# Kernel optimization log

Measured on AMD Instinct MI355X. Metric: run time of the kernel, lower is better.

## Reference

```python
import jax, jax.numpy as jnp
import numpy as np

B, S, T, D, V = 512, 128, 128, 512, 128  # batch, enc len, dec steps (=longest_smi), dim_model, output_size


def setup_inputs() -> dict:
    key = jax.random.key(0)
    ks = jax.random.split(key, 17)
    sc = 0.05
    return {
        "e_all": jax.random.normal(ks[0], (B, S, D), jnp.float32),
        "e_h": jax.random.normal(ks[1], (1, B, D), jnp.float32),
        "e_c": jax.random.normal(ks[2], (1, B, D), jnp.float32),
        "target": jax.random.randint(ks[3], (B, T), 0, T),
        # params (Linear weights stored [in, out], y = x @ W + b)
        "E": jax.random.normal(ks[4], (T, D), jnp.float32) * sc,        # Embedding(longest_smi, D)
        "Wa": jax.random.normal(ks[5], (D, D), jnp.float32) * sc,
        "ba": jnp.zeros((D,), jnp.float32),
        "Ua": jax.random.normal(ks[6], (D, D), jnp.float32) * sc,
        "bu": jnp.zeros((D,), jnp.float32),
        "Va": jax.random.normal(ks[7], (D, 1), jnp.float32) * sc,
        "bv": jnp.zeros((1,), jnp.float32),
        "W_ih": jax.random.normal(ks[8], (2 * D, 4 * D), jnp.float32) * sc,
        "b_ih": jnp.zeros((4 * D,), jnp.float32),
        "W_hh": jax.random.normal(ks[9], (D, 4 * D), jnp.float32) * sc,
        "b_hh": jnp.zeros((4 * D,), jnp.float32),
        "W_out": jax.random.normal(ks[10], (D, V), jnp.float32) * sc,
        "b_out": jnp.zeros((V,), jnp.float32),
    }


def reference(e_all, e_h, e_c, target, E, Wa, ba, Ua, bu, Va, bv,
              W_ih, b_ih, W_hh, b_hh, W_out, b_out):
    Bb = e_all.shape[0]
    # teacher forcing: step 0 input is token 0 (SOS), then target[:, :-1]
    idx = jnp.concatenate([jnp.zeros((Bb, 1), target.dtype), target[:, :-1]], axis=1)  # [B,T]
    emb_all = E[idx]                       # [B,T,D] (dropout is identity in eval)
    keys_proj = e_all @ Ua + bu            # Ua(keys), loop-invariant  [B,S,D]
    h0, c0 = e_h[0], e_c[0]                # [B,D]

    def step(carry, emb):
        h, c = carry
        q = (h + c) @ Wa + ba                                   # [B,D]  Wa(query)
        s = jnp.tanh(q[:, None, :] + keys_proj) @ Va + bv       # [B,S,1]
        w = jax.nn.softmax(s[..., 0], axis=-1)                  # [B,S]
        ctx = jnp.einsum('bs,bsd->bd', w, e_all)                # [B,D]
        x = jnp.concatenate([emb, ctx], axis=-1)                # [B,2D]
        g = x @ W_ih + b_ih + h @ W_hh + b_hh                   # [B,4D], torch gate order i,f,g,o
        i_, f_, g_, o_ = jnp.split(g, 4, axis=-1)
        c2 = jax.nn.sigmoid(f_) * c + jax.nn.sigmoid(i_) * jnp.tanh(g_)
        h2 = jax.nn.sigmoid(o_) * jnp.tanh(c2)
        out = h2 @ W_out + b_out                                # [B,V]
        return (h2, c2), (out, w)

    _, (outs, attns) = jax.lax.scan(step, (h0, c0), jnp.swapaxes(emb_all, 0, 1))
    outputs = jax.nn.log_softmax(jnp.swapaxes(outs, 0, 1), axis=-1)  # [B,T,V]
    cross_attn = jnp.swapaxes(attns, 0, 1)                           # [B,T,S]
    return outputs, cross_attn
```

## Files before the change

kernel.cpp:

```cpp
#include <hip/hip_runtime.h>

#define B_ 512
#define S_ 128
#define T_ 128
#define D_ 512
#define V_ 128
#define LDW 72

typedef __attribute__((ext_vector_type(8))) short s16x8;
typedef __attribute__((ext_vector_type(4))) short s16x4;
typedef __attribute__((ext_vector_type(4))) float f32x4;

__device__ __forceinline__ float b2f(unsigned short h) {
    union { unsigned int u; float f; } x; x.u = ((unsigned int)h) << 16; return x.f;
}
__device__ __forceinline__ unsigned short f2b(float f) {
    union { float f; unsigned int u; } x; x.f = f;
    unsigned int u = x.u; u += 0x7FFFu + ((u >> 16) & 1u);
    return (unsigned short)(u >> 16);
}
#if __has_builtin(__builtin_amdgcn_rcpf)
__device__ __forceinline__ float rcp_f(float x) { return __builtin_amdgcn_rcpf(x); }
#else
__device__ __forceinline__ float rcp_f(float x) { return 1.0f / x; }
#endif
__device__ __forceinline__ float sigm(float x) { return rcp_f(1.0f + __expf(-x)); }
__device__ __forceinline__ float tanh_fast(float x) {
    float e = __expf(2.0f * fabsf(x));
    float r = 1.0f - 2.0f * rcp_f(e + 1.0f);
    return copysignf(r, x);
}
__device__ __forceinline__ float tanh_pade(float x) {
    float t = x * x;
    float num = x * fmaf(t, 105.0f + t, 945.0f);
    float den = fmaf(t, fmaf(t, 15.0f, 420.0f), 945.0f);
    float r = num * rcp_f(den);
    return fminf(1.0f, fmaxf(-1.0f, r));
}

#if __has_builtin(__builtin_amdgcn_cvt_f32_fp8)
__device__ __forceinline__ f32x4 fp8x4_dec(unsigned w) {
    f32x4 r;
    r[0] = __builtin_amdgcn_cvt_f32_fp8(w, 0);
    r[1] = __builtin_amdgcn_cvt_f32_fp8(w, 1);
    r[2] = __builtin_amdgcn_cvt_f32_fp8(w, 2);
    r[3] = __builtin_amdgcn_cvt_f32_fp8(w, 3);
    return r;
}
#else
__device__ __forceinline__ float fp8_dec_sw(unsigned w, int j) {
    unsigned char v = (w >> (8 * j)) & 0xFF;
    unsigned s = v >> 7, e = (v >> 3) & 0xF, m = v & 7;
    float r = (e == 0) ? ldexpf((float)m, -9) : ldexpf((float)(8 + m), (int)e - 10);
    return s ? -r : r;
}
__device__ __forceinline__ f32x4 fp8x4_dec(unsigned w) {
    f32x4 r;
    r[0] = fp8_dec_sw(w, 0); r[1] = fp8_dec_sw(w, 1);
    r[2] = fp8_dec_sw(w, 2); r[3] = fp8_dec_sw(w, 3);
    return r;
}
#endif

#if __has_builtin(__builtin_amdgcn_cvt_pk_fp8_f32)
__device__ __forceinline__ unsigned pk_fp8(float a, float b, float c, float d) {
    int r = 0;
    r = __builtin_amdgcn_cvt_pk_fp8_f32(a, b, r, false);
    r = __builtin_amdgcn_cvt_pk_fp8_f32(c, d, r, true);
    return (unsigned)r;
}
#else
__device__ __forceinline__ unsigned char f32_to_fp8_sw(float x) {
    unsigned s = x < 0.f ? 0x80u : 0u; float a = fabsf(x);
    if (a != a) return (unsigned char)(s | 0x7F);
    if (a >= 448.f) return (unsigned char)(s | 0x7E);
    if (a < 0.001953125f) { int m = (int)rintf(a * 512.0f); return (unsigned char)(s | (m > 7 ? 0x08 : m)); }
    int e; float fr = frexpf(a, &e);
    int m = (int)rintf(fr * 16.0f - 8.0f);
    int ee = e - 1 + 7;
    if (m == 8) { m = 0; ee += 1; }
    if (ee <= 0) { int mm = (int)rintf(a * 512.f); return (unsigned char)(s | (mm > 7 ? 0x08 : mm)); }
    if (ee >= 16) return (unsigned char)(s | 0x7E);
    return (unsigned char)(s | (ee << 3) | m);
}
__device__ __forceinline__ unsigned pk_fp8(float a, float b, float c, float d) {
    return (unsigned)f32_to_fp8_sw(a) | ((unsigned)f32_to_fp8_sw(b) << 8)
         | ((unsigned)f32_to_fp8_sw(c) << 16) | ((unsigned)f32_to_fp8_sw(d) << 24);
}
#endif

struct P {
    const int* target;
    const float* E; const float* bv; const float* ba; const float* bout;
    const short* vab;
    const unsigned char* ea8; const unsigned char* kp8;
    const short* WaT; const short* WehT; const short* WctxT; const short* WoutT;
    const float* bcat;
    short* qbf; short* xeh; short* ctxb; short* gpA; short* gpB;
    short* hcbf; short* h2bf; float* cst;
    float* out_logits; float* out_attn;
};

struct AttnS { float scp[4][64]; float wbuf[S_]; float cpart[4][D_]; };
struct OutS  { short As[64][LDW]; short Bs[128][LDW]; };
struct PG2   { short As[128][LDW]; short Bs[64][LDW]; };
struct GateS { short As[64][LDW]; short Bs[64][LDW]; float gt[64][65]; };
union SharedC { OutS o; PG2 g; };

__device__ __forceinline__ void attn_phase(const P& p, AttnS& sh, int b, int step)
{
    const int t = threadIdx.x, lane = t & 63, wave = t >> 6;
    {
        const int sg = wave & 1, dh = wave >> 1;
        const int s = sg * 64 + lane;
        const unsigned char* kb = p.kp8 + (size_t)b * (S_ * D_);
        const short* qv = p.qbf + (size_t)b * D_;
        float acc = 0.f;
        #pragma unroll 4
        for (int i = 0; i < 16; ++i) {
            int g = dh * 16 + i;
            uint4 kw = *(const uint4*)(kb + ((size_t)g * 128 + s) * 16);
            const short* qg = qv + g * 16;
            const short* vg = p.vab + g * 16;
            s16x8 q0 = *(const s16x8*)(qg), q1 = *(const s16x8*)(qg + 8);
            s16x8 v0 = *(const s16x8*)(vg), v1 = *(const s16x8*)(vg + 8);
            f32x4 ka = fp8x4_dec(kw.x), kb4 = fp8x4_dec(kw.y);
            f32x4 kc = fp8x4_dec(kw.z), kd = fp8x4_dec(kw.w);
            #pragma unroll
            for (int j = 0; j < 4; ++j) {
                acc += tanh_pade(b2f((unsigned short)q0[j])     + ka[j])  * b2f((unsigned short)v0[j]);
                acc += tanh_pade(b2f((unsigned short)q0[4 + j]) + kb4[j]) * b2f((unsigned short)v0[4 + j]);
                acc += tanh_pade(b2f((unsigned short)q1[j])     + kc[j])  * b2f((unsigned short)v1[j]);
                acc += tanh_pade(b2f((unsigned short)q1[4 + j]) + kd[j])  * b2f((unsigned short)v1[4 + j]);
            }
        }
        sh.scp[wave][lane] = acc;
    }
    __syncthreads();
    if (wave == 0) {
        const float bvv = p.bv[0];
        float v0 = sh.scp[0][lane] + sh.scp[2][lane] + bvv;
        float v1 = sh.scp[1][lane] + sh.scp[3][lane] + bvv;
        float m = fmaxf(v0, v1);
        #pragma unroll
        for (int o = 32; o >= 1; o >>= 1) m = fmaxf(m, __shfl_xor(m, o));
        float e0 = __expf(v0 - m), e1 = __expf(v1 - m);
        float su = e0 + e1;
        #pragma unroll
        for (int o = 32; o >= 1; o >>= 1) su += __shfl_xor(su, o);
        float inv = rcp_f(su);
        float w0 = e0 * inv, w1 = e1 * inv;
        sh.wbuf[lane] = w0; sh.wbuf[lane + 64] = w1;
        float* ao = p.out_attn + ((size_t)b * T_ + step) * S_;
        ao[lane] = w0; ao[lane + 64] = w1;
    }
    __syncthreads();
    {
        const int d0 = lane * 8;
        f32x4 aA = {0.f,0.f,0.f,0.f}, aB = {0.f,0.f,0.f,0.f};
        const unsigned char* eb = p.ea8 + (size_t)b * S_ * D_ + d0;
        #pragma unroll 4
        for (int i = 0; i < 32; ++i) {
            int s = wave * 32 + i;
            float wv = sh.wbuf[s];
            uint2 ev = *(const uint2*)(eb + (size_t)s * D_);
            f32x4 ex = fp8x4_dec(ev.x), ey = fp8x4_dec(ev.y);
            #pragma unroll
            for (int j = 0; j < 4; ++j) aA[j] += wv * ex[j];
            #pragma unroll
            for (int j = 0; j < 4; ++j) aB[j] += wv * ey[j];
        }
        *(f32x4*)&sh.cpart[wave][d0]     = aA;
        *(f32x4*)&sh.cpart[wave][d0 + 4] = aB;
    }
    __syncthreads();
    {
        int dd = t * 2;
        float v0 = sh.cpart[0][dd]   + sh.cpart[1][dd]   + sh.cpart[2][dd]   + sh.cpart[3][dd];
        float v1 = sh.cpart[0][dd+1] + sh.cpart[1][dd+1] + sh.cpart[2][dd+1] + sh.cpart[3][dd+1];
        short2 o2; o2.x = (short)f2b(v0); o2.y = (short)f2b(v1);
        *(short2*)(p.ctxb + (size_t)b * D_ + dd) = o2;
    }
}

__device__ __forceinline__ void pgate_phase(const P& p, PG2& sh, int bid2, int koff,
                                            short* __restrict__ gpp, bool addb)
{
    const int t = threadIdx.x, lane = t & 63, wave = t >> 6;
    const int lrow = lane & 15, kq = lane >> 4;
    const int m0 = (bid2 >> 5) * 128, n0 = (bid2 & 31) * 64;
    f32x4 acc[2][4] = {};
    for (int k0 = 0; k0 < 512; k0 += 64) {
        s16x8 va[4], vb[2];
        #pragma unroll
        for (int r = 0; r < 4; ++r) {
            int idx = r * 256 + t, row = idx >> 3, seg = idx & 7;
            va[r] = *(const s16x8*)(p.xeh + (size_t)(m0 + row) * 1024 + koff + k0 + seg * 8);
        }
        #pragma unroll
        for (int r = 0; r < 2; ++r) {
            int idx = r * 256 + t, row = idx >> 3, seg = idx & 7;
            vb[r] = *(const s16x8*)(p.WehT + (size_t)(n0 + row) * 1024 + koff + k0 + seg * 8);
        }
        __syncthreads();
        #pragma unroll
        for (int r = 0; r < 4; ++r) {
            int idx = r * 256 + t, row = idx >> 3, seg = idx & 7;
            *(s16x8*)(&sh.As[row][seg * 8]) = va[r];
        }
        #pragma unroll
        for (int r = 0; r < 2; ++r) {
            int idx = r * 256 + t, row = idx >> 3, seg = idx & 7;
            *(s16x8*)(&sh.Bs[row][seg * 8]) = vb[r];
        }
        __syncthreads();
        #pragma unroll
        for (int kk = 0; kk < 64; kk += 32) {
            s16x8 af[2], bf[4];
            af[0] = *(const s16x8*)(&sh.As[wave * 32 + lrow][kk + kq * 8]);
            af[1] = *(const s16x8*)(&sh.As[wave * 32 + 16 + lrow][kk + kq * 8]);
            #pragma unroll
            for (int f = 0; f < 4; ++f)
                bf[f] = *(const s16x8*)(&sh.Bs[f * 16 + lrow][kk + kq * 8]);
            #pragma unroll
            for (int m2 = 0; m2 < 2; ++m2)
                #pragma unroll
                for (int n2 = 0; n2 < 4; ++n2)
                    acc[m2][n2] = __builtin_amdgcn_mfma_f32_16x16x32_bf16(af[m2], bf[n2], acc[m2][n2], 0, 0, 0);
        }
    }
    #pragma unroll
    for (int m2 = 0; m2 < 2; ++m2)
        #pragma unroll
        for (int n2 = 0; n2 < 4; ++n2) {
            int col = n0 + n2 * 16 + lrow;
            float bvv = addb ? p.bcat[col] : 0.0f;
            #pragma unroll
            for (int j = 0; j < 4; ++j) {
                int row = m0 + wave * 32 + m2 * 16 + kq * 4 + j;
                gpp[(size_t)row * 2048 + col] = (short)f2b(acc[m2][n2][j] + bvv);
            }
        }
}

__device__ __forceinline__ void fgate_phase(const P& p, GateS& sh, int bid, int step)
{
    const int t = threadIdx.x, lane = t & 63, wave = t >> 6;
    const int wr = wave >> 1, wc = wave & 1;
    const int lrow = lane & 15, kq = lane >> 4;
    const int srow = t >> 3, sseg = t & 7;
    const int m0 = (bid >> 5) * 64, n0 = (bid & 31) * 64;
    f32x4 acc[2][2] = {};
    for (int k0 = 0; k0 < 512; k0 += 64) {
        s16x8 va0 = *(const s16x8*)(p.ctxb + (size_t)(m0 + srow) * 512 + k0 + sseg * 8);
        s16x8 va1 = *(const s16x8*)(p.ctxb + (size_t)(m0 + srow + 32) * 512 + k0 + sseg * 8);
        s16x8 vb0 = *(const s16x8*)(p.WctxT + (size_t)(n0 + srow) * 512 + k0 + sseg * 8);
        s16x8 vb1 = *(const s16x8*)(p.WctxT + (size_t)(n0 + srow + 32) * 512 + k0 + sseg * 8);
        __syncthreads();
        *(s16x8*)(&sh.As[srow][sseg * 8]) = va0;
        *(s16x8*)(&sh.As[srow + 32][sseg * 8]) = va1;
        *(s16x8*)(&sh.Bs[srow][sseg * 8]) = vb0;
        *(s16x8*)(&sh.Bs[srow + 32][sseg * 8]) = vb1;
        __syncthreads();
        #pragma unroll
        for (int kk = 0; kk < 64; kk += 32) {
            s16x8 af0 = *(const s16x8*)(&sh.As[wr * 32 + lrow][kk + kq * 8]);
            s16x8 af1 = *(const s16x8*)(&sh.As[wr * 32 + 16 + lrow][kk + kq * 8]);
            s16x8 bf0 = *(const s16x8*)(&sh.Bs[wc * 32 + lrow][kk + kq * 8]);
            s16x8 bf1 = *(const s16x8*)(&sh.Bs[wc * 32 + 16 + lrow][kk + kq * 8]);
            acc[0][0] = __builtin_amdgcn_mfma_f32_16x16x32_bf16(af0, bf0, acc[0][0], 0, 0, 0);
            acc[0][1] = __builtin_amdgcn_mfma_f32_16x16x32_bf16(af0, bf1, acc[0][1], 0, 0, 0);
            acc[1][0] = __builtin_amdgcn_mfma_f32_16x16x32_bf16(af1, bf0, acc[1][0], 0, 0, 0);
            acc[1][1] = __builtin_amdgcn_mfma_f32_16x16x32_bf16(af1, bf1, acc[1][1], 0, 0, 0);
        }
    }
    #pragma unroll
    for (int m2 = 0; m2 < 2; ++m2)
        #pragma unroll
        for (int n2 = 0; n2 < 2; ++n2) {
            int cl = wc * 32 + n2 * 16 + lrow;
            #pragma unroll
            for (int j = 0; j < 4; ++j) {
                int rl = wr * 32 + m2 * 16 + kq * 4 + j;
                size_t gidx = (size_t)(m0 + rl) * 2048 + n0 + cl;
                sh.gt[rl][cl] = acc[m2][n2][j]
                              + b2f((unsigned short)p.gpA[gidx])
                              + b2f((unsigned short)p.gpB[gidx]);
            }
        }
    __syncthreads();
    const int rl4 = t >> 4, dl = t & 15;
    #pragma unroll
    for (int pass = 0; pass < 4; ++pass) {
        int row = pass * 16 + rl4;
        int b = m0 + row;
        int d = (n0 >> 2) + dl;
        float gi = sh.gt[row][dl * 4 + 0];
        float gf = sh.gt[row][dl * 4 + 1];
        float gg = sh.gt[row][dl * 4 + 2];
        float go = sh.gt[row][dl * 4 + 3];
        float cv = p.cst[(size_t)b * D_ + d];
        float c2 = sigm(gf) * cv + sigm(gi) * tanh_fast(gg);
        float h2 = sigm(go) * tanh_fast(c2);
        p.cst[(size_t)b * D_ + d] = c2;
        p.hcbf[(size_t)b * D_ + d] = (short)f2b(h2 + c2);
        p.h2bf[(size_t)b * D_ + d] = (short)f2b(h2);
        p.xeh[(size_t)b * 1024 + 512 + d] = (short)f2b(h2);
        int tok = p.target[b * T_ + step];
        p.xeh[(size_t)b * 1024 + d] = (short)f2b(p.E[(size_t)tok * D_ + d]);
    }
}

__device__ __forceinline__ void q_phase(const P& p, OutS& sh, int bid)
{
    const int t = threadIdx.x, lane = t & 63, wave = t >> 6;
    const int lrow = lane & 15, kq = lane >> 4;
    const int srow = t >> 3, sseg = t & 7;
    const int m0 = (bid >> 4) * 64, n0 = (bid & 15) * 32;
    f32x4 acc0 = {}, acc1 = {};
    for (int k0 = 0; k0 < 512; k0 += 64) {
        s16x8 va0 = *(const s16x8*)(p.hcbf + (size_t)(m0 + srow) * 512 + k0 + sseg * 8);
        s16x8 va1 = *(const s16x8*)(p.hcbf + (size_t)(m0 + srow + 32) * 512 + k0 + sseg * 8);
        int brow = n0 + (srow & 31);
        s16x8 vb0 = *(const s16x8*)(p.WaT + (size_t)brow * 512 + k0 + sseg * 8);
        __syncthreads();
        *(s16x8*)(&sh.As[srow][sseg * 8]) = va0;
        *(s16x8*)(&sh.As[srow + 32][sseg * 8]) = va1;
        if (srow < 32) *(s16x8*)(&sh.Bs[srow][sseg * 8]) = vb0;
        __syncthreads();
        #pragma unroll
        for (int kk = 0; kk < 64; kk += 32) {
            s16x8 af  = *(const s16x8*)(&sh.As[wave * 16 + lrow][kk + kq * 8]);
            s16x8 bf0 = *(const s16x8*)(&sh.Bs[lrow][kk + kq * 8]);
            s16x8 bf1 = *(const s16x8*)(&sh.Bs[16 + lrow][kk + kq * 8]);
            acc0 = __builtin_amdgcn_mfma_f32_16x16x32_bf16(af, bf0, acc0, 0, 0, 0);
            acc1 = __builtin_amdgcn_mfma_f32_16x16x32_bf16(af, bf1, acc1, 0, 0, 0);
        }
    }
    #pragma unroll
    for (int n2 = 0; n2 < 2; ++n2) {
        int col = n0 + n2 * 16 + lrow;
        float bvv = p.ba[col];
        f32x4 av = n2 ? acc1 : acc0;
        #pragma unroll
        for (int j = 0; j < 4; ++j) {
            int row = m0 + wave * 16 + kq * 4 + j;
            p.qbf[(size_t)row * 512 + col] = (short)f2b(av[j] + bvv);
        }
    }
}

__device__ __forceinline__ void out_phase(const P& p, OutS& sh, int obid, int step)
{
    const int t = threadIdx.x, lane = t & 63, wave = t >> 6;
    const int lrow = lane & 15, kq = lane >> 4;
    const int srow = t >> 3, sseg = t & 7;
    const int m0 = obid * 64;
    f32x4 acc[8] = {};
    for (int k0 = 0; k0 < 512; k0 += 64) {
        s16x8 va0 = *(const s16x8*)(p.h2bf + (size_t)(m0 + srow) * 512 + k0 + sseg * 8);
        s16x8 va1 = *(const s16x8*)(p.h2bf + (size_t)(m0 + srow + 32) * 512 + k0 + sseg * 8);
        s16x8 vb[4];
        #pragma unroll
        for (int p4 = 0; p4 < 4; ++p4)
            vb[p4] = *(const s16x8*)(p.WoutT + (size_t)(srow + p4 * 32) * 512 + k0 + sseg * 8);
        __syncthreads();
        *(s16x8*)(&sh.As[srow][sseg * 8]) = va0;
        *(s16x8*)(&sh.As[srow + 32][sseg * 8]) = va1;
        #pragma unroll
        for (int p4 = 0; p4 < 4; ++p4) *(s16x8*)(&sh.Bs[srow + p4 * 32][sseg * 8]) = vb[p4];
        __syncthreads();
        #pragma unroll
        for (int kk = 0; kk < 64; kk += 32) {
            s16x8 a = *(const s16x8*)(&sh.As[wave * 16 + lrow][kk + kq * 8]);
            #pragma unroll
            for (int f = 0; f < 8; ++f) {
                s16x8 b = *(const s16x8*)(&sh.Bs[f * 16 + lrow][kk + kq * 8]);
                acc[f] = __builtin_amdgcn_mfma_f32_16x16x32_bf16(a, b, acc[f], 0, 0, 0);
            }
        }
    }
    float colb[8];
    #pragma unroll
    for (int f = 0; f < 8; ++f) colb[f] = p.bout[f * 16 + lrow];
    #pragma unroll
    for (int j = 0; j < 4; ++j) {
        float v[8]; float mx = -1e30f;
        #pragma unroll
        for (int f = 0; f < 8; ++f) { v[f] = acc[f][j] + colb[f]; mx = fmaxf(mx, v[f]); }
        #pragma unroll
        for (int o = 1; o < 16; o <<= 1) mx = fmaxf(mx, __shfl_xor(mx, o));
        float sum = 0.f;
        #pragma unroll
        for (int f = 0; f < 8; ++f) sum += __expf(v[f] - mx);
        #pragma unroll
        for (int o = 1; o < 16; o <<= 1) sum += __shfl_xor(sum, o);
        float lse = mx + __logf(sum);
        int row = m0 + wave * 16 + kq * 4 + j;
        float* orow = p.out_logits + ((size_t)row * T_ + step) * V_;
        #pragma unroll
        for (int f = 0; f < 8; ++f) orow[f * 16 + lrow] = v[f] - lse;
    }
}

__global__ __launch_bounds__(256, 2) void kA(P p, int step) {
    __shared__ AttnS sh;
    attn_phase(p, sh, blockIdx.x, step);
}
__global__ __launch_bounds__(256, 2) void kB(P p, int step) {
    __shared__ GateS sh;
    fgate_phase(p, sh, blockIdx.x, step);
}
template<bool INIT>
__global__ __launch_bounds__(256, 2) void kC(P p, int step) {
    __shared__ SharedC sh;
    const int bid = blockIdx.x;
    if (bid < 128)       q_phase(p, sh.o, bid);
    else if (bid < 256)  pgate_phase(p, sh.g, bid - 128, 0,   p.gpA, true);
    else if (bid < 384)  pgate_phase(p, sh.g, bid - 256, 512, p.gpB, false);
    else if (!INIT)      out_phase(p, sh.o, bid - 384, step);
}

__global__ __launch_bounds__(256)
void gemm64(const short* __restrict__ A, const short* __restrict__ Bt,
            const float* __restrict__ bias, short* __restrict__ Cp,
            int M, int N, int K)
{
    __shared__ __align__(16) short As[64][LDW];
    __shared__ __align__(16) short Bs[64][LDW];
    const int t = threadIdx.x;
    const int lane = t & 63, wave = t >> 6;
    const int wr = wave >> 1, wc = wave & 1;
    const int lrow = lane & 15, kq = lane >> 4;
    const int m0 = blockIdx.y * 64, n0 = blockIdx.x * 64;
    const int srow = t >> 3, sseg = t & 7;
    f32x4 acc[2][2] = {};
    for (int k0 = 0; k0 < K; k0 += 64) {
        s16x8 va0 = *(const s16x8*)(A + (size_t)(m0 + srow) * K + k0 + sseg * 8);
        s16x8 va1 = *(const s16x8*)(A + (size_t)(m0 + srow + 32) * K + k0 + sseg * 8);
        s16x8 vb0 = *(const s16x8*)(Bt + (size_t)(n0 + srow) * K + k0 + sseg * 8);
        s16x8 vb1 = *(const s16x8*)(Bt + (size_t)(n0 + srow + 32) * K + k0 + sseg * 8);
        __syncthreads();
        *(s16x8*)(&As[srow][sseg * 8]) = va0;
        *(s16x8*)(&As[srow + 32][sseg * 8]) = va1;
        *(s16x8*)(&Bs[srow][sseg * 8]) = vb0;
        *(s16x8*)(&Bs[srow + 32][sseg * 8]) = vb1;
        __syncthreads();
        for (int kk = 0; kk < 64; kk += 32) {
            s16x8 af[2], bf[2];
            af[0] = *(const s16x8*)(&As[wr * 32 + lrow][kk + kq * 8]);
            af[1] = *(const s16x8*)(&As[wr * 32 + 16 + lrow][kk + kq * 8]);
            bf[0] = *(const s16x8*)(&Bs[wc * 32 + lrow][kk + kq * 8]);
            bf[1] = *(const s16x8*)(&Bs[wc * 32 + 16 + lrow][kk + kq * 8]);
            for (int m2 = 0; m2 < 2; ++m2)
                for (int n2 = 0; n2 < 2; ++n2)
                    acc[m2][n2] = __builtin_amdgcn_mfma_f32_16x16x32_bf16(af[m2], bf[n2], acc[m2][n2], 0, 0, 0);
        }
    }
    for (int m2 = 0; m2 < 2; ++m2)
        for (int n2 = 0; n2 < 2; ++n2) {
            int col = n0 + wc * 32 + n2 * 16 + lrow;
            float bvv = bias ? bias[col] : 0.0f;
            for (int j = 0; j < 4; ++j) {
                int row = m0 + wr * 32 + m2 * 16 + kq * 4 + j;
                Cp[(size_t)row * N + col] = (short)f2b(acc[m2][n2][j] + bvv);
            }
        }
}

__global__ __launch_bounds__(256)
void transpose_kp8(const short* __restrict__ in, unsigned char* __restrict__ out)
{
    const int b = blockIdx.x, t = threadIdx.x;
    const size_t ibase = (size_t)b * (S_ * D_);
    for (int k = t; k < 32 * S_; k += 256) {
        int g = k >> 7, s = k & 127;
        const short* src = in + ibase + (size_t)s * D_ + g * 16;
        unsigned w[4];
        #pragma unroll
        for (int q4 = 0; q4 < 4; ++q4) {
            w[q4] = pk_fp8(b2f((unsigned short)src[q4 * 4 + 0]), b2f((unsigned short)src[q4 * 4 + 1]),
                           b2f((unsigned short)src[q4 * 4 + 2]), b2f((unsigned short)src[q4 * 4 + 3]));
        }
        uint4 o; o.x = w[0]; o.y = w[1]; o.z = w[2]; o.w = w[3];
        *(uint4*)(out + ibase + ((size_t)g * S_ + s) * 16) = o;
    }
}

__global__ __launch_bounds__(256)
void cast_fp8_v4(const float* __restrict__ in, unsigned char* __restrict__ out, int n4)
{
    int i = blockIdx.x * 256 + threadIdx.x;
    int stride = gridDim.x * 256;
    for (; i < n4; i += stride) {
        f32x4 v = ((const f32x4*)in)[i];
        ((unsigned*)out)[i] = pk_fp8(v[0], v[1], v[2], v[3]);
    }
}

__global__ __launch_bounds__(256)
void init_state(const float* __restrict__ e_h, const float* __restrict__ e_c,
                float* __restrict__ c, short* __restrict__ hcbf,
                short* __restrict__ xeh, const float* __restrict__ E)
{
    int gid = blockIdx.x * 256 + threadIdx.x;
    int b = gid >> 9, d = gid & 511;
    float h0 = e_h[gid], c0 = e_c[gid];
    c[gid] = c0;
    hcbf[gid] = (short)f2b(h0 + c0);
    xeh[(size_t)b * 1024 + 512 + d] = (short)f2b(h0);
    xeh[(size_t)b * 1024 + d] = (short)f2b(E[d]);
}

__global__ __launch_bounds__(256)
void transpose_cast(const float* __restrict__ in, short* __restrict__ out,
                    int N, int ostride, int koff, int gate_perm)
{
    __shared__ float tile[64][65];
    int t = threadIdx.x;
    int n0 = blockIdx.x * 64, k0 = blockIdx.y * 64;
    int cc = t & 63, r4 = t >> 6;
    for (int i = 0; i < 16; ++i) {
        int r = i * 4 + r4;
        tile[r][cc] = in[(size_t)(k0 + r) * N + n0 + cc];
    }
    __syncthreads();
    for (int i = 0; i < 16; ++i) {
        int nr = i * 4 + r4;
        int ng = n0 + nr;
        int np = gate_perm ? ((ng & 511) * 4 + (ng >> 9)) : ng;
        out[(size_t)np * ostride + koff + k0 + cc] = (short)f2b(tile[cc][nr]);
    }
}

__global__ __launch_bounds__(256)
void cast_bf16_v4(const float* __restrict__ in, short* __restrict__ out, int n4)
{
    int i = blockIdx.x * 256 + threadIdx.x;
    int stride = gridDim.x * 256;
    for (; i < n4; i += stride) {
        f32x4 v = ((const f32x4*)in)[i];
        s16x4 o;
        for (int j = 0; j < 4; ++j) o[j] = (short)f2b(v[j]);
        ((s16x4*)out)[i] = o;
    }
}

__global__ __launch_bounds__(256)
void make_bcat(const float* __restrict__ b_ih, const float* __restrict__ b_hh, float* __restrict__ bcat)
{
    int i = blockIdx.x * 256 + threadIdx.x;
    if (i < 2048) {
        int np = (i & 511) * 4 + (i >> 9);
        bcat[np] = b_ih[i] + b_hh[i];
    }
}

extern "C" void kernel_launch(void* const* d_in, const int* in_sizes, int n_in,
                              void* d_out, int out_size, void* d_ws, size_t ws_size,
                              hipStream_t stream)
{
    const float* e_all  = (const float*)d_in[0];
    const float* e_h    = (const float*)d_in[1];
    const float* e_c    = (const float*)d_in[2];
    const int*   target = (const int*)d_in[3];
    const float* E      = (const float*)d_in[4];
    const float* Wa     = (const float*)d_in[5];
    const float* ba     = (const float*)d_in[6];
    const float* Ua     = (const float*)d_in[7];
    const float* bu     = (const float*)d_in[8];
    const float* Va     = (const float*)d_in[9];
    const float* bv     = (const float*)d_in[10];
    const float* W_ih   = (const float*)d_in[11];
    const float* b_ih   = (const float*)d_in[12];
    const float* W_hh   = (const float*)d_in[13];
    const float* b_hh   = (const float*)d_in[14];
    const float* W_out  = (const float*)d_in[15];
    const float* b_out  = (const float*)d_in[16];

    char* ws = (char*)d_ws;
    size_t off = 0;
    auto alloc = [&](size_t bytes) { void* p = ws + off; off += (bytes + 255) & ~255ull; return p; };
    short* ealb  = (short*)alloc((size_t)B_ * S_ * D_ * 2);
    short* kpb   = (short*)alloc((size_t)B_ * S_ * D_ * 2);
    unsigned char* kp8 = (unsigned char*)alloc((size_t)B_ * S_ * D_);
    unsigned char* ea8 = (unsigned char*)alloc((size_t)B_ * S_ * D_);
    short* WaT   = (short*)alloc((size_t)D_ * D_ * 2);
    short* UaT   = (short*)alloc((size_t)D_ * D_ * 2);
    short* WehT  = (short*)alloc((size_t)2048 * 1024 * 2);
    short* WctxT = (short*)alloc((size_t)2048 * 512 * 2);
    short* WoutT = (short*)alloc((size_t)V_ * D_ * 2);
    float* bcat  = (float*)alloc(2048 * 4);
    short* qbf   = (short*)alloc((size_t)B_ * D_ * 2);
    short* vab   = (short*)alloc((size_t)D_ * 2);
    short* xeh   = (short*)alloc((size_t)B_ * 1024 * 2);
    short* ctxb  = (short*)alloc((size_t)B_ * D_ * 2);
    short* gpA   = (short*)alloc((size_t)B_ * 2048 * 2);
    short* gpB   = (short*)alloc((size_t)B_ * 2048 * 2);
    short* hcbf  = (short*)alloc((size_t)B_ * D_ * 2);
    short* h2bf  = (short*)alloc((size_t)B_ * D_ * 2);
    float* cst   = (float*)alloc((size_t)B_ * D_ * 4);
    if (off > ws_size) return;

    float* out_logits = (float*)d_out;
    float* out_attn   = (float*)d_out + (size_t)B_ * T_ * V_;

    cast_bf16_v4<<<4096, 256, 0, stream>>>(e_all, ealb, B_ * S_ * D_ / 4);
    cast_fp8_v4<<<4096, 256, 0, stream>>>(e_all, ea8, B_ * S_ * D_ / 4);
    cast_bf16_v4<<<1,    256, 0, stream>>>(Va, vab, D_ / 4);
    transpose_cast<<<dim3(8, 8),  256, 0, stream>>>(Wa,  WaT,  512,  512, 0, 0);
    transpose_cast<<<dim3(8, 8),  256, 0, stream>>>(Ua,  UaT,  512,  512, 0, 0);
    transpose_cast<<<dim3(32, 8), 256, 0, stream>>>(W_ih,              WehT,  2048, 1024, 0,   1);
    transpose_cast<<<dim3(32, 8), 256, 0, stream>>>(W_ih + 512 * 2048, WctxT, 2048, 512,  0,   1);
    transpose_cast<<<dim3(32, 8), 256, 0, stream>>>(W_hh,              WehT,  2048, 1024, 512, 1);
    transpose_cast<<<dim3(2, 8),  256, 0, stream>>>(W_out, WoutT, 128, 512, 0, 0);
    make_bcat<<<8, 256, 0, stream>>>(b_ih, b_hh, bcat);
    gemm64<<<dim3(8, 1024), 256, 0, stream>>>(ealb, UaT, bu, kpb, B_ * S_, 512, 512);
    transpose_kp8<<<512, 256, 0, stream>>>(kpb, kp8);
    init_state<<<1024, 256, 0, stream>>>(e_h, e_c, cst, hcbf, xeh, E);

    P pp;
    pp.target = target; pp.E = E; pp.bv = bv; pp.ba = ba; pp.bout = b_out;
    pp.vab = vab;
    pp.ea8 = ea8; pp.kp8 = kp8; pp.WaT = WaT; pp.WehT = WehT; pp.WctxT = WctxT; pp.WoutT = WoutT;
    pp.bcat = bcat; pp.qbf = qbf; pp.xeh = xeh; pp.ctxb = ctxb; pp.gpA = gpA; pp.gpB = gpB;
    pp.hcbf = hcbf; pp.h2bf = h2bf; pp.cst = cst;
    pp.out_logits = out_logits; pp.out_attn = out_attn;

    kC<true><<<384, 256, 0, stream>>>(pp, 0);

    for (int t = 0; t < T_; ++t) {
        kA<<<512, 256, 0, stream>>>(pp, t);
        kB<<<256, 256, 0, stream>>>(pp, t);
        kC<false><<<392, 256, 0, stream>>>(pp, t);
    }
    (void)n_in; (void)in_sizes; (void)out_size;
}
```

Before: 6.259 ms.

## Fuse gate and post-gate kernels with per-row-group atomic flags

Merges the final gate kernel and the q/pre-gate/output kernel into one launch per step. Consumer blocks spin-wait on per-row-group atomic counters that the gate blocks set once their rows are written. Pre-gates are now a single K=1024 GEMM written to ping-pong buffers, and the q GEMM uses 64x64 tiles. This removes one launch and a grid-wide barrier per step, but relies on producer blocks being scheduled before waiting consumers to avoid deadlock.

```diff
diff --git a/kernel.cpp b/kernel.cpp
--- a/kernel.cpp
+++ b/kernel.cpp
@@ -91,24 +91,42 @@
 
 struct P {
     const int* target;
-    const float* E; const float* bv; const float* ba; const float* bout;
+    const float* E; const float* bv; const float* ba; const float* bout; const float* bcat;
     const short* vab;
     const unsigned char* ea8; const unsigned char* kp8;
     const short* WaT; const short* WehT; const short* WctxT; const short* WoutT;
-    const float* bcat;
-    short* qbf; short* xeh; short* ctxb; short* gpA; short* gpB;
-    short* hcbf; short* h2bf; float* cst;
+    short* qbf; short* ctxb; short* gp0; short* gp1;
+    float* cst; short* hcbf; short* h2bf; short* xeh;
+    unsigned* flags;
     float* out_logits; float* out_attn;
 };
 
-struct AttnS { float scp[4][64]; float wbuf[S_]; float cpart[4][D_]; };
+struct GateS { short As[64][LDW]; short Bs[64][LDW]; float gt[64][65]; };
+struct PG2   { short As[128][LDW]; short Bs[64][LDW]; };
 struct OutS  { short As[64][LDW]; short Bs[128][LDW]; };
-struct PG2   { short As[128][LDW]; short Bs[64][LDW]; };
-struct GateS { short As[64][LDW]; short Bs[64][LDW]; float gt[64][65]; };
-union SharedC { OutS o; PG2 g; };
-
-__device__ __forceinline__ void attn_phase(const P& p, AttnS& sh, int b, int step)
-{
+union SharedBC { GateS g; PG2 pg; OutS o; };
+
+__device__ __forceinline__ void signal_flag(unsigned* f) {
+    __syncthreads();
+    __threadfence();
+    if (threadIdx.x == 0)
+        __hip_atomic_fetch_add(f, 1u, __ATOMIC_RELAXED, __HIP_MEMORY_SCOPE_AGENT);
+}
+__device__ __forceinline__ void wait_flag(unsigned* f, unsigned tgt) {
+    if (threadIdx.x == 0) {
+        while (__hip_atomic_load(f, __ATOMIC_RELAXED, __HIP_MEMORY_SCOPE_AGENT) < tgt)
+            __builtin_amdgcn_s_sleep(2);
+    }
+    __syncthreads();
+    __threadfence();
+}
+
+__global__ __launch_bounds__(256, 2) void kA(P p, int step)
+{
+    __shared__ float scp[4][64];
+    __shared__ float wbuf[S_];
+    __shared__ float cpart[4][D_];
+    const int b = blockIdx.x;
     const int t = threadIdx.x, lane = t & 63, wave = t >> 6;
     {
         const int sg = wave & 1, dh = wave >> 1;
@@ -134,13 +152,13 @@
                 acc += tanh_pade(b2f((unsigned short)q1[4 + j]) + kd[j])  * b2f((unsigned short)v1[4 + j]);
             }
         }
-        sh.scp[wave][lane] = acc;
+        scp[wave][lane] = acc;
     }
     __syncthreads();
     if (wave == 0) {
         const float bvv = p.bv[0];
-        float v0 = sh.scp[0][lane] + sh.scp[2][lane] + bvv;
-        float v1 = sh.scp[1][lane] + sh.scp[3][lane] + bvv;
+        float v0 = scp[0][lane] + scp[2][lane] + bvv;
+        float v1 = scp[1][lane] + scp[3][lane] + bvv;
         float m = fmaxf(v0, v1);
         #pragma unroll
         for (int o = 32; o >= 1; o >>= 1) m = fmaxf(m, __shfl_xor(m, o));
@@ -150,7 +168,7 @@
         for (int o = 32; o >= 1; o >>= 1) su += __shfl_xor(su, o);
         float inv = rcp_f(su);
         float w0 = e0 * inv, w1 = e1 * inv;
-        sh.wbuf[lane] = w0; sh.wbuf[lane + 64] = w1;
+        wbuf[lane] = w0; wbuf[lane + 64] = w1;
         float* ao = p.out_attn + ((size_t)b * T_ + step) * S_;
         ao[lane] = w0; ao[lane + 64] = w1;
     }
@@ -162,7 +180,7 @@
         #pragma unroll 4
         for (int i = 0; i < 32; ++i) {
             int s = wave * 32 + i;
-            float wv = sh.wbuf[s];
+            float wv = wbuf[s];
             uint2 ev = *(const uint2*)(eb + (size_t)s * D_);
             f32x4 ex = fp8x4_dec(ev.x), ey = fp8x4_dec(ev.y);
             #pragma unroll
@@ -170,80 +188,21 @@
             #pragma unroll
             for (int j = 0; j < 4; ++j) aB[j] += wv * ey[j];
         }
-        *(f32x4*)&sh.cpart[wave][d0]     = aA;
-        *(f32x4*)&sh.cpart[wave][d0 + 4] = aB;
+        *(f32x4*)&cpart[wave][d0]     = aA;
+        *(f32x4*)&cpart[wave][d0 + 4] = aB;
     }
     __syncthreads();
     {
         int dd = t * 2;
-        float v0 = sh.cpart[0][dd]   + sh.cpart[1][dd]   + sh.cpart[2][dd]   + sh.cpart[3][dd];
-        float v1 = sh.cpart[0][dd+1] + sh.cpart[1][dd+1] + sh.cpart[2][dd+1] + sh.cpart[3][dd+1];
+        float v0 = cpart[0][dd]   + cpart[1][dd]   + cpart[2][dd]   + cpart[3][dd];
+        float v1 = cpart[0][dd+1] + cpart[1][dd+1] + cpart[2][dd+1] + cpart[3][dd+1];
         short2 o2; o2.x = (short)f2b(v0); o2.y = (short)f2b(v1);
         *(short2*)(p.ctxb + (size_t)b * D_ + dd) = o2;
     }
 }
 
-__device__ __forceinline__ void pgate_phase(const P& p, PG2& sh, int bid2, int koff,
-                                            short* __restrict__ gpp, bool addb)
-{
-    const int t = threadIdx.x, lane = t & 63, wave = t >> 6;
-    const int lrow = lane & 15, kq = lane >> 4;
-    const int m0 = (bid2 >> 5) * 128, n0 = (bid2 & 31) * 64;
-    f32x4 acc[2][4] = {};
-    for (int k0 = 0; k0 < 512; k0 += 64) {
-        s16x8 va[4], vb[2];
-        #pragma unroll
-        for (int r = 0; r < 4; ++r) {
-            int idx = r * 256 + t, row = idx >> 3, seg = idx & 7;
-            va[r] = *(const s16x8*)(p.xeh + (size_t)(m0 + row) * 1024 + koff + k0 + seg * 8);
-        }
-        #pragma unroll
-        for (int r = 0; r < 2; ++r) {
-            int idx = r * 256 + t, row = idx >> 3, seg = idx & 7;
-            vb[r] = *(const s16x8*)(p.WehT + (size_t)(n0 + row) * 1024 + koff + k0 + seg * 8);
-        }
-        __syncthreads();
-        #pragma unroll
-        for (int r = 0; r < 4; ++r) {
-            int idx = r * 256 + t, row = idx >> 3, seg = idx & 7;
-            *(s16x8*)(&sh.As[row][seg * 8]) = va[r];
-        }
-        #pragma unroll
-        for (int r = 0; r < 2; ++r) {
-            int idx = r * 256 + t, row = idx >> 3, seg = idx & 7;
-            *(s16x8*)(&sh.Bs[row][seg * 8]) = vb[r];
-        }
-        __syncthreads();
-        #pragma unroll
-        for (int kk = 0; kk < 64; kk += 32) {
-            s16x8 af[2], bf[4];
-            af[0] = *(const s16x8*)(&sh.As[wave * 32 + lrow][kk + kq * 8]);
-            af[1] = *(const s16x8*)(&sh.As[wave * 32 + 16 + lrow][kk + kq * 8]);
-            #pragma unroll
-            for (int f = 0; f < 4; ++f)
-                bf[f] = *(const s16x8*)(&sh.Bs[f * 16 + lrow][kk + kq * 8]);
-            #pragma unroll
-            for (int m2 = 0; m2 < 2; ++m2)
-                #pragma unroll
-                for (int n2 = 0; n2 < 4; ++n2)
-                    acc[m2][n2] = __builtin_amdgcn_mfma_f32_16x16x32_bf16(af[m2], bf[n2], acc[m2][n2], 0, 0, 0);
-        }
-    }
-    #pragma unroll
-    for (int m2 = 0; m2 < 2; ++m2)
-        #pragma unroll
-        for (int n2 = 0; n2 < 4; ++n2) {
-            int col = n0 + n2 * 16 + lrow;
-            float bvv = addb ? p.bcat[col] : 0.0f;
-            #pragma unroll
-            for (int j = 0; j < 4; ++j) {
-                int row = m0 + wave * 32 + m2 * 16 + kq * 4 + j;
-                gpp[(size_t)row * 2048 + col] = (short)f2b(acc[m2][n2][j] + bvv);
-            }
-        }
-}
-
-__device__ __forceinline__ void fgate_phase(const P& p, GateS& sh, int bid, int step)
+__device__ __forceinline__ void fgate_phase(const P& p, GateS& sh, int bid, int step,
+                                            const short* __restrict__ gprd)
 {
     const int t = threadIdx.x, lane = t & 63, wave = t >> 6;
     const int wr = wave >> 1, wc = wave & 1;
@@ -282,10 +241,8 @@
             #pragma unroll
             for (int j = 0; j < 4; ++j) {
                 int rl = wr * 32 + m2 * 16 + kq * 4 + j;
-                size_t gidx = (size_t)(m0 + rl) * 2048 + n0 + cl;
                 sh.gt[rl][cl] = acc[m2][n2][j]
-                              + b2f((unsigned short)p.gpA[gidx])
-                              + b2f((unsigned short)p.gpB[gidx]);
+                              + b2f((unsigned short)gprd[(size_t)(m0 + rl) * 2048 + n0 + cl]);
             }
         }
     __syncthreads();
@@ -311,43 +268,108 @@
     }
 }
 
-__device__ __forceinline__ void q_phase(const P& p, OutS& sh, int bid)
+__device__ __forceinline__ void q64_phase(const P& p, OutS& sh, int bid)
 {
     const int t = threadIdx.x, lane = t & 63, wave = t >> 6;
+    const int wr = wave >> 1, wc = wave & 1;
     const int lrow = lane & 15, kq = lane >> 4;
     const int srow = t >> 3, sseg = t & 7;
-    const int m0 = (bid >> 4) * 64, n0 = (bid & 15) * 32;
-    f32x4 acc0 = {}, acc1 = {};
+    const int m0 = (bid >> 3) * 64, n0 = (bid & 7) * 64;
+    f32x4 acc[2][2] = {};
     for (int k0 = 0; k0 < 512; k0 += 64) {
         s16x8 va0 = *(const s16x8*)(p.hcbf + (size_t)(m0 + srow) * 512 + k0 + sseg * 8);
         s16x8 va1 = *(const s16x8*)(p.hcbf + (size_t)(m0 + srow + 32) * 512 + k0 + sseg * 8);
-        int brow = n0 + (srow & 31);
-        s16x8 vb0 = *(const s16x8*)(p.WaT + (size_t)brow * 512 + k0 + sseg * 8);
+        s16x8 vb0 = *(const s16x8*)(p.WaT + (size_t)(n0 + srow) * 512 + k0 + sseg * 8);
+        s16x8 vb1 = *(const s16x8*)(p.WaT + (size_t)(n0 + srow + 32) * 512 + k0 + sseg * 8);
         __syncthreads();
         *(s16x8*)(&sh.As[srow][sseg * 8]) = va0;
         *(s16x8*)(&sh.As[srow + 32][sseg * 8]) = va1;
-        if (srow < 32) *(s16x8*)(&sh.Bs[srow][sseg * 8]) = vb0;
+        *(s16x8*)(&sh.Bs[srow][sseg * 8]) = vb0;
+        *(s16x8*)(&sh.Bs[srow + 32][sseg * 8]) = vb1;
         __syncthreads();
         #pragma unroll
         for (int kk = 0; kk < 64; kk += 32) {
-            s16x8 af  = *(const s16x8*)(&sh.As[wave * 16 + lrow][kk + kq * 8]);
-            s16x8 bf0 = *(const s16x8*)(&sh.Bs[lrow][kk + kq * 8]);
-            s16x8 bf1 = *(const s16x8*)(&sh.Bs[16 + lrow][kk + kq * 8]);
-            acc0 = __builtin_amdgcn_mfma_f32_16x16x32_bf16(af, bf0, acc0, 0, 0, 0);
-            acc1 = __builtin_amdgcn_mfma_f32_16x16x32_bf16(af, bf1, acc1, 0, 0, 0);
+            s16x8 af0 = *(const s16x8*)(&sh.As[wr * 32 + lrow][kk + kq * 8]);
+            s16x8 af1 = *(const s16x8*)(&sh.As[wr * 32 + 16 + lrow][kk + kq * 8]);
+            s16x8 bf0 = *(const s16x8*)(&sh.Bs[wc * 32 + lrow][kk + kq * 8]);
+            s16x8 bf1 = *(const s16x8*)(&sh.Bs[wc * 32 + 16 + lrow][kk + kq * 8]);
+            acc[0][0] = __builtin_amdgcn_mfma_f32_16x16x32_bf16(af0, bf0, acc[0][0], 0, 0, 0);
+            acc[0][1] = __builtin_amdgcn_mfma_f32_16x16x32_bf16(af0, bf1, acc[0][1], 0, 0, 0);
+            acc[1][0] = __builtin_amdgcn_mfma_f32_16x16x32_bf16(af1, bf0, acc[1][0], 0, 0, 0);
+            acc[1][1] = __builtin_amdgcn_mfma_f32_16x16x32_bf16(af1, bf1, acc[1][1], 0, 0, 0);
         }
     }
     #pragma unroll
-    for (int n2 = 0; n2 < 2; ++n2) {
-        int col = n0 + n2 * 16 + lrow;
-        float bvv = p.ba[col];
-        f32x4 av = n2 ? acc1 : acc0;
-        #pragma unroll
-        for (int j = 0; j < 4; ++j) {
-            int row = m0 + wave * 16 + kq * 4 + j;
-            p.qbf[(size_t)row * 512 + col] = (short)f2b(av[j] + bvv);
-        }
-    }
+    for (int m2 = 0; m2 < 2; ++m2)
+        #pragma unroll
+        for (int n2 = 0; n2 < 2; ++n2) {
+            int col = n0 + wc * 32 + n2 * 16 + lrow;
+            float bvv = p.ba[col];
+            #pragma unroll
+            for (int j = 0; j < 4; ++j) {
+                int row = m0 + wr * 32 + m2 * 16 + kq * 4 + j;
+                p.qbf[(size_t)row * 512 + col] = (short)f2b(acc[m2][n2][j] + bvv);
+            }
+        }
+}
+
+__device__ __forceinline__ void pgate_full(const P& p, PG2& sh, int bid2, short* __restrict__ gpw)
+{
+    const int t = threadIdx.x, lane = t & 63, wave = t >> 6;
+    const int lrow = lane & 15, kq = lane >> 4;
+    const int m0 = (bid2 >> 5) * 128, n0 = (bid2 & 31) * 64;
+    f32x4 acc[2][4] = {};
+    for (int k0 = 0; k0 < 1024; k0 += 64) {
+        s16x8 va[4], vb[2];
+        #pragma unroll
+        for (int r = 0; r < 4; ++r) {
+            int idx = r * 256 + t, row = idx >> 3, seg = idx & 7;
+            va[r] = *(const s16x8*)(p.xeh + (size_t)(m0 + row) * 1024 + k0 + seg * 8);
+        }
+        #pragma unroll
+        for (int r = 0; r < 2; ++r) {
+            int idx = r * 256 + t, row = idx >> 3, seg = idx & 7;
+            vb[r] = *(const s16x8*)(p.WehT + (size_t)(n0 + row) * 1024 + k0 + seg * 8);
+        }
+        __syncthreads();
+        #pragma unroll
+        for (int r = 0; r < 4; ++r) {
+            int idx = r * 256 + t, row = idx >> 3, seg = idx & 7;
+            *(s16x8*)(&sh.As[row][seg * 8]) = va[r];
+        }
+        #pragma unroll
+        for (int r = 0; r < 2; ++r) {
+            int idx = r * 256 + t, row = idx >> 3, seg = idx & 7;
+            *(s16x8*)(&sh.Bs[row][seg * 8]) = vb[r];
+        }
+        __syncthreads();
+        #pragma unroll
+        for (int kk = 0; kk < 64; kk += 32) {
+            s16x8 af[2], bf[4];
+            af[0] = *(const s16x8*)(&sh.As[wave * 32 + lrow][kk + kq * 8]);
+            af[1] = *(const s16x8*)(&sh.As[wave * 32 + 16 + lrow][kk + kq * 8]);
+            #pragma unroll
+            for (int f = 0; f < 4; ++f)
+                bf[f] = *(const s16x8*)(&sh.Bs[f * 16 + lrow][kk + kq * 8]);
+            #pragma unroll
+            for (int m2 = 0; m2 < 2; ++m2)
+                #pragma unroll
+                for (int n2 = 0; n2 < 4; ++n2)
+                    acc[m2][n2] = __builtin_amdgcn_mfma_f32_16x16x32_bf16(af[m2], bf[n2], acc[m2][n2], 0, 0, 0);
+        }
+    }
+    #pragma unroll
+    for (int m2 = 0; m2 < 2; ++m2)
+        #pragma unroll
+        for (int n2 = 0; n2 < 4; ++n2) {
+            int col = n0 + n2 * 16 + lrow;
+            float bvv = p.bcat[col];
+            #pragma unroll
+            for (int j = 0; j < 4; ++j) {
+                int row = m0 + wave * 32 + m2 * 16 + kq * 4 + j;
+                gpw[(size_t)row * 2048 + col] = (short)f2b(acc[m2][n2][j] + bvv);
+            }
+        }
 }
 
 __device__ __forceinline__ void out_phase(const P& p, OutS& sh, int obid, int step)
@@ -403,22 +425,45 @@
     }
 }
 
-__global__ __launch_bounds__(256, 2) void kA(P p, int step) {
-    __shared__ AttnS sh;
-    attn_phase(p, sh, blockIdx.x, step);
-}
-__global__ __launch_bounds__(256, 2) void kB(P p, int step) {
-    __shared__ GateS sh;
-    fgate_phase(p, sh, blockIdx.x, step);
-}
-template<bool INIT>
-__global__ __launch_bounds__(256, 2) void kC(P p, int step) {
-    __shared__ SharedC sh;
+__global__ __launch_bounds__(256, 2) void kBC(P p, int step)
+{
+    __shared__ SharedBC sh;
     const int bid = blockIdx.x;
-    if (bid < 128)       q_phase(p, sh.o, bid);
-    else if (bid < 256)  pgate_phase(p, sh.g, bid - 128, 0,   p.gpA, true);
-    else if (bid < 384)  pgate_phase(p, sh.g, bid - 256, 512, p.gpB, false);
-    else if (!INIT)      out_phase(p, sh.o, bid - 384, step);
+    unsigned* fl = p.flags + step * 8;
+    short* gprd = (step & 1) ? p.gp1 : p.gp0;
+    short* gpwr = (step & 1) ? p.gp0 : p.gp1;
+    if (bid < 256) {
+        fgate_phase(p, sh.g, bid, step, gprd);
+        signal_flag(&fl[bid >> 5]);
+    } else if (bid < 320) {
+        int qb = bid - 256;
+        wait_flag(&fl[qb >> 3], 32);
+        q64_phase(p, sh.o, qb);
+    } else if (bid < 448) {
+        int pb = bid - 320;
+        int mg = (pb >> 5) * 2;
+        wait_flag(&fl[mg], 32);
+        wait_flag(&fl[mg + 1], 32);
+        pgate_full(p, sh.pg, pb, gpwr);
+    } else {
+        int ob = bid - 448;
+        wait_flag(&fl[ob], 32);
+        out_phase(p, sh.o, ob, step);
+    }
+}
+
+__global__ __launch_bounds__(256, 2) void kInit(P p)
+{
+    __shared__ SharedBC sh;
+    const int bid = blockIdx.x;
+    if (bid < 64) q64_phase(p, sh.o, bid);
+    else          pgate_full(p, sh.pg, bid - 64, p.gp0);
+}
+
+__global__ __launch_bounds__(256) void zero_flags(unsigned* f, int n)
+{
+    int i = blockIdx.x * 256 + threadIdx.x;
+    if (i < n) f[i] = 0;
 }
 
 __global__ __launch_bounds__(256)
@@ -595,16 +640,18 @@
     short* vab   = (short*)alloc((size_t)D_ * 2);
     short* xeh   = (short*)alloc((size_t)B_ * 1024 * 2);
     short* ctxb  = (short*)alloc((size_t)B_ * D_ * 2);
-    short* gpA   = (short*)alloc((size_t)B_ * 2048 * 2);
-    short* gpB   = (short*)alloc((size_t)B_ * 2048 * 2);
+    short* gp0   = (short*)alloc((size_t)B_ * 2048 * 2);
+    short* gp1   = (short*)alloc((size_t)B_ * 2048 * 2);
     short* hcbf  = (short*)alloc((size_t)B_ * D_ * 2);
     short* h2bf  = (short*)alloc((size_t)B_ * D_ * 2);
     float* cst   = (float*)alloc((size_t)B_ * D_ * 4);
+    unsigned* flags = (unsigned*)alloc((size_t)T_ * 8 * 4);
     if (off > ws_size) return;
 
     float* out_logits = (float*)d_out;
     float* out_attn   = (float*)d_out + (size_t)B_ * T_ * V_;
 
+    zero_flags<<<4, 256, 0, stream>>>(flags, T_ * 8);
     cast_bf16_v4<<<4096, 256, 0, stream>>>(e_all, ealb, B_ * S_ * D_ / 4);
     cast_fp8_v4<<<4096, 256, 0, stream>>>(e_all, ea8, B_ * S_ * D_ / 4);
     cast_bf16_v4<<<1,    256, 0, stream>>>(Va, vab, D_ / 4);
@@ -620,19 +667,19 @@
     init_state<<<1024, 256, 0, stream>>>(e_h, e_c, cst, hcbf, xeh, E);
 
     P pp;
-    pp.target = target; pp.E = E; pp.bv = bv; pp.ba = ba; pp.bout = b_out;
-    pp.vab = vab;
-    pp.ea8 = ea8; pp.kp8 = kp8; pp.WaT = WaT; pp.WehT = WehT; pp.WctxT = WctxT; pp.WoutT = WoutT;
-    pp.bcat = bcat; pp.qbf = qbf; pp.xeh = xeh; pp.ctxb = ctxb; pp.gpA = gpA; pp.gpB = gpB;
-    pp.hcbf = hcbf; pp.h2bf = h2bf; pp.cst = cst;
+    pp.target = target; pp.E = E; pp.bv = bv; pp.ba = ba; pp.bout = b_out; pp.bcat = bcat;
+    pp.vab = vab; pp.ea8 = ea8; pp.kp8 = kp8;
+    pp.WaT = WaT; pp.WehT = WehT; pp.WctxT = WctxT; pp.WoutT = WoutT;
+    pp.qbf = qbf; pp.ctxb = ctxb; pp.gp0 = gp0; pp.gp1 = gp1;
+    pp.cst = cst; pp.hcbf = hcbf; pp.h2bf = h2bf; pp.xeh = xeh;
+    pp.flags = flags;
     pp.out_logits = out_logits; pp.out_attn = out_attn;
 
-    kC<true><<<384, 256, 0, stream>>>(pp, 0);
+    kInit<<<192, 256, 0, stream>>>(pp);
 
     for (int t = 0; t < T_; ++t) {
         kA<<<512, 256, 0, stream>>>(pp, t);
-        kB<<<256, 256, 0, stream>>>(pp, t);
-        kC<false><<<392, 256, 0, stream>>>(pp, t);
+        kBC<<<456, 256, 0, stream>>>(pp, t);
     }
     (void)n_in; (void)in_sizes; (void)out_size;
 }
```

Result: slower. 15.07 ms (+140.7%).
